# Performance work log

Measured on AMD Instinct MI355X. Metric: run time of the kernel, lower is better.

Reference implementation:

```python
import jax, jax.numpy as jnp
import numpy as np

N, E, IN, H, B, R, ND, K, ER = 50000, 800000, 256, 256, 256, 8, 5000, 16, 20000
LAM = 0.7


def _gat(x, src, dst, W, a_src, a_dst, b):
    """Single-head PyG-style GATConv, add_self_loops=False."""
    h = x @ W                                   # [N,H]
    s = (h @ a_src)[src] + (h @ a_dst)[dst]     # [E]
    e = jax.nn.leaky_relu(s, 0.2)
    m = jax.ops.segment_max(e, dst, num_segments=N)
    m = jnp.where(jnp.isneginf(m), 0.0, m)
    p = jnp.exp(e - m[dst])
    z = jax.ops.segment_sum(p, dst, num_segments=N)
    alpha = p / (z[dst] + 1e-16)                # softmax over incoming edges
    out = jax.ops.segment_sum(alpha[:, None] * h[src], dst, num_segments=N)
    return out + b


def setup_inputs() -> dict:
    key = jax.random.key(0)
    ks = jax.random.split(key, 20)
    d = {}
    d['x'] = jax.random.normal(ks[0], (N, IN), dtype=jnp.float32)
    d['edge_index'] = jax.random.randint(ks[1], (2, E), 0, N)
    d['head_indices'] = jax.random.randint(ks[2], (B,), 0, N)
    d['rel_types'] = jax.random.randint(ks[3], (B,), 0, R)
    d['tail_indices'] = jax.random.randint(ks[4], (B,), 0, N)
    d['g2l'] = jax.random.randint(ks[5], (N,), 0, ND)
    d['rel_edge_src'] = jax.random.randint(ks[6], (3, ER), 0, ND)
    d['sim_neighbors'] = jax.random.randint(ks[7], (ND, K), 0, N)
    d['sim_weights'] = jax.random.uniform(ks[8], (ND, K), dtype=jnp.float32) / K
    sc1 = 1.0 / np.sqrt(IN)
    sc2 = 1.0 / np.sqrt(H)
    d['W1'] = jax.random.normal(ks[9], (IN, H), dtype=jnp.float32) * sc1
    d['a1_src'] = jax.random.normal(ks[10], (H,), dtype=jnp.float32) * sc2
    d['a1_dst'] = jax.random.normal(ks[11], (H,), dtype=jnp.float32) * sc2
    d['b1'] = jnp.zeros((H,), dtype=jnp.float32)
    d['W2'] = jax.random.normal(ks[12], (H, H), dtype=jnp.float32) * sc2
    d['a2_src'] = jax.random.normal(ks[13], (H,), dtype=jnp.float32) * sc2
    d['a2_dst'] = jax.random.normal(ks[14], (H,), dtype=jnp.float32) * sc2
    d['b2'] = jnp.zeros((H,), dtype=jnp.float32)
    d['rel_emb'] = jax.random.normal(ks[15], (R, H), dtype=jnp.float32) * sc2
    return d


def reference(x, edge_index, head_indices, rel_types, tail_indices, g2l,
              rel_edge_src, sim_neighbors, sim_weights,
              W1, a1_src, a1_dst, b1, W2, a2_src, a2_dst, b2, rel_emb):
    src, dst = edge_index[0], edge_index[1]
    # Encoder: GAT -> SiLU -> GAT
    h = _gat(x, src, dst, W1, a1_src, a1_dst, b1)
    h = jax.nn.silu(h)
    node_emb = _gat(h, src, dst, W2, a2_src, a2_dst, b2)  # [N,H]

    # Sequential per-triplet disease-embedding modification (rel 4/5/6)
    def step(emb, tr):
        hi, r = tr
        is_dis = (r >= 4) & (r <= 6)
        ridx = jnp.clip(r - 4, 0, 2)
        local = g2l[hi]
        deg = jnp.sum(rel_edge_src[ridx] == local).astype(emb.dtype)
        c = LAM * jnp.exp(-LAM * deg) + 0.2
        nb = sim_neighbors[local]           # [K]
        w = sim_weights[local]              # [K]
        vec = (w[:, None] * emb[nb]).sum(0)  # weighted neighbor mix
        new = c * vec + (1.0 - c) * emb[hi]
        row = jnp.where(is_dis, new, emb[hi])
        return emb.at[hi].set(row), None

    node_emb, _ = jax.lax.scan(step, node_emb, (head_indices, rel_types))

    # DistMult decode
    head = node_emb[head_indices]
    tail = node_emb[tail_indices]
    rel = rel_emb[rel_types]
    score = (head * rel * tail).sum(-1)
    return jax.nn.sigmoid(score)
```

## Files before the change

### kernel.cpp

```cpp
#include <hip/hip_runtime.h>
#include <cstdint>

#define N_NODES 50000
#define N_EDGES 800000
#define DIM     256
#define BSZ     256
#define ND_     5000
#define KNB     16
#define ER_     20000
#define LAM     0.7f

typedef unsigned int uint;
typedef unsigned short ushort;
typedef __attribute__((ext_vector_type(8))) short bf16x8;
typedef __attribute__((ext_vector_type(4))) float f32x4;

#define MTILES_PAD 3128
#define NB_SCAN    ((N_NODES + 255) / 256)

__device__ __forceinline__ ushort f2bf(float f) {
    uint u = __float_as_uint(f);
    uint r = u + 0x7FFFu + ((u >> 16) & 1u);
    return (ushort)(r >> 16);
}
__device__ __forceinline__ float bflo(uint u) { return __uint_as_float(u << 16); }
__device__ __forceinline__ float bfhi(uint u) { return __uint_as_float(u & 0xffff0000u); }


__device__ __forceinline__ bf16x8 make_af_f32(const float* __restrict__ A,
                                              int row, int c0, int M) {
    float4 v0 = make_float4(0.f, 0.f, 0.f, 0.f);
    float4 v1 = make_float4(0.f, 0.f, 0.f, 0.f);
    if (row < M) {
        v0 = *(const float4*)(A + (size_t)row * 256 + c0);
        v1 = *(const float4*)(A + (size_t)row * 256 + c0 + 16);
    }
    uint4 o;
    o.x = (uint)f2bf(v0.x) | ((uint)f2bf(v0.y) << 16);
    o.y = (uint)f2bf(v0.z) | ((uint)f2bf(v0.w) << 16);
    o.z = (uint)f2bf(v1.x) | ((uint)f2bf(v1.y) << 16);
    o.w = (uint)f2bf(v1.z) | ((uint)f2bf(v1.w) << 16);
    return *(bf16x8*)&o;
}
__device__ __forceinline__ bf16x8 make_af_bf16(const ushort* __restrict__ A,
                                               int row, int c0, int M) {
    uint2 v0 = make_uint2(0u, 0u), v1 = make_uint2(0u, 0u);
    if (row < M) {
        v0 = *(const uint2*)(A + (size_t)row * 256 + c0);
        v1 = *(const uint2*)(A + (size_t)row * 256 + c0 + 16);
    }
    uint4 o; o.x = v0.x; o.y = v0.y; o.z = v1.x; o.w = v1.y;
    return *(bf16x8*)&o;
}

__global__ __launch_bounds__(256)
void pack_b_kernel(const float* __restrict__ W, ushort* __restrict__ out) {
    const int nt = blockIdx.x;
    const int t  = threadIdx.x;
    const int l  = t & 63;
    const int kt0 = (t >> 6) * 2;
    const int n  = nt * 16 + (l & 15);
    const int lg = l >> 4;
#pragma unroll
    for (int p = 0; p < 2; ++p) {
        int kt = kt0 + p;
        ushort us[8];
#pragma unroll
        for (int j = 0; j < 8; ++j) {
            int kk = (j & 3) + lg * 4 + (j >> 2) * 16;
            us[j] = f2bf(W[(size_t)(kt * 32 + kk) * 256 + n]);
        }
        ushort* dst = out + ((size_t)(nt * 8 + kt) * 64 + l) * 8;
        *(uint4*)dst = *(uint4*)us;
    }
}

template<int SRCF32>
__global__ __launch_bounds__(256)
void gemm_bf16_kernel(const float* __restrict__ Af, const ushort* __restrict__ Ab,
                      const ushort* __restrict__ Bp, ushort* __restrict__ H,
                      const float* __restrict__ a_src, const float* __restrict__ a_dst,
                      float* __restrict__ hs, float* __restrict__ hd, int M) {
    __shared__ float sdS[4][64];
    __shared__ float sdD[4][64];
    const int t = threadIdx.x;
    const int w = t >> 6;
    const int l = t & 63;
    const int mt0 = blockIdx.x * 4;
    const int cb  = (l & 15);
    const int lg  = l >> 4;
    f32x4 acc[4][4];
#pragma unroll
    for (int i = 0; i < 4; ++i)
#pragma unroll
        for (int j = 0; j < 4; ++j) acc[i][j] = (f32x4){0.f, 0.f, 0.f, 0.f};

    for (int kt = 0; kt < 8; ++kt) {
        bf16x8 af[4], bfr[4];
        const int c0 = kt * 32 + lg * 4;
#pragma unroll
        for (int mi = 0; mi < 4; ++mi) {
            int row = (mt0 + mi) * 16 + cb;
            af[mi] = SRCF32 ? make_af_f32(Af, row, c0, M)
                            : make_af_bf16(Ab, row, c0, M);
        }
#pragma unroll
        for (int ni = 0; ni < 4; ++ni)
            bfr[ni] = *(const bf16x8*)(Bp + ((size_t)((w * 4 + ni) * 8 + kt) * 64 + l) * 8);
#pragma unroll
        for (int mi = 0; mi < 4; ++mi)
#pragma unroll
            for (int ni = 0; ni < 4; ++ni)
                acc[mi][ni] = __builtin_amdgcn_mfma_f32_16x16x32_bf16(
                    af[mi], bfr[ni], acc[mi][ni], 0, 0, 0);
    }
    const int rbase = (l >> 4) * 4;
    float asv[4], adv[4];
#pragma unroll
    for (int ni = 0; ni < 4; ++ni) {
        int col = (w * 4 + ni) * 16 + cb;
        asv[ni] = a_src[col];
        adv[ni] = a_dst[col];
    }
#pragma unroll
    for (int mi = 0; mi < 4; ++mi) {
#pragma unroll
        for (int r = 0; r < 4; ++r) {
            int row = (mt0 + mi) * 16 + rbase + r;
            float ps = 0.f, pd = 0.f;
#pragma unroll
            for (int ni = 0; ni < 4; ++ni) {
                float hv = acc[mi][ni][r];
                ps = fmaf(hv, asv[ni], ps);
                pd = fmaf(hv, adv[ni], pd);
                if (row < M) {
                    int col = (w * 4 + ni) * 16 + cb;
                    H[(size_t)row * 256 + col] = f2bf(hv);
                }
            }
#pragma unroll
            for (int o = 1; o < 16; o <<= 1) {
                ps += __shfl_xor(ps, o);
                pd += __shfl_xor(pd, o);
            }
            if (cb == 0) {
                sdS[w][mi * 16 + rbase + r] = ps;
                sdD[w][mi * 16 + rbase + r] = pd;
            }
        }
    }
    __syncthreads();
    if (t < 64) {
        int row = mt0 * 16 + t;
        if (row < M) {
            hs[row] = sdS[0][t] + sdS[1][t] + sdS[2][t] + sdS[3][t];
            hd[row] = sdD[0][t] + sdD[1][t] + sdD[2][t] + sdD[3][t];
        }
    }
}

__global__ __launch_bounds__(256)
void hist_kernel(const int* __restrict__ ei, int* __restrict__ deg) {
    int e = blockIdx.x * 256 + threadIdx.x;
    if (e < N_EDGES) atomicAdd(&deg[ei[N_EDGES + e]], 1);
}

__global__ __launch_bounds__(256)
void blockscan_kernel(const int* __restrict__ deg, int* __restrict__ off,
                      int* __restrict__ bsum) {
    __shared__ int s[256];
    const int b = blockIdx.x, t = threadIdx.x;
    const int idx = b * 256 + t;
    int v = (idx < N_NODES) ? deg[idx] : 0;
    s[t] = v;
    __syncthreads();
    for (int o = 1; o < 256; o <<= 1) {
        int x = (t >= o) ? s[t - o] : 0;
        __syncthreads();
        s[t] += x;
        __syncthreads();
    }
    if (idx < N_NODES) off[idx] = s[t] - v;
    if (t == 255) bsum[b] = s[255];
}

__global__ __launch_bounds__(256)
void scan_bsum_kernel(const int* __restrict__ bsum, int* __restrict__ bpre) {
    __shared__ int s[256];
    const int t = threadIdx.x;
    int v = (t < NB_SCAN) ? bsum[t] : 0;
    s[t] = v;
    __syncthreads();
    for (int o = 1; o < 256; o <<= 1) {
        int x = (t >= o) ? s[t - o] : 0;
        __syncthreads();
        s[t] += x;
        __syncthreads();
    }
    if (t < NB_SCAN) bpre[t] = s[t] - v;
}

__global__ __launch_bounds__(256)
void add_offsets_kernel(int* __restrict__ off, const int* __restrict__ bpre) {
    const int b = blockIdx.x, t = threadIdx.x;
    const int idx = b * 256 + t;
    if (idx < N_NODES) off[idx] += bpre[b];
}

__global__ __launch_bounds__(256)
void scatter_kernel(const int* __restrict__ ei, int* __restrict__ off,
                    int* __restrict__ csr_src) {
    int e = blockIdx.x * 256 + threadIdx.x;
    if (e >= N_EDGES) return;
    int d = ei[N_EDGES + e];
    int pos = atomicAdd(&off[d], 1);
    csr_src[pos] = ei[e];
}

__global__ __launch_bounds__(256)
void gat_aggr_kernel(const int* __restrict__ off, const int* __restrict__ csr_src,
                     const float* __restrict__ hs, const float* __restrict__ hd,
                     const ushort* __restrict__ hb, const float* __restrict__ bias,
                     float* __restrict__ out_f32, ushort* __restrict__ out_bf,
                     int do_silu) {
    const int d = blockIdx.x * 4 + (threadIdx.x >> 6);
    const int l = threadIdx.x & 63;
    if (d >= N_NODES) return;
    const int beg = d ? off[d - 1] : 0;
    const int end = off[d];
    const float hdd = hd[d];

    float acc0 = 0.f, acc1 = 0.f, acc2 = 0.f, acc3 = 0.f;
    float zl = 0.f;
    const ushort* __restrict__ hcol = hb + l * 4;

    for (int c0 = beg; c0 < end; c0 += 64) {
        const int cn = min(end - c0, 64);
        int s = 0; float pexp = 0.f;
        if (l < cn) {
            s = csr_src[c0 + l];
            float v = hs[s] + hdd;
            v = (v >= 0.f) ? v : 0.2f * v;
            pexp = __expf(v);
        }
        zl += pexp;
        const int nb4 = cn & ~3;
        int j = 0;
        if (nb4) {
            int s0 = __shfl(s, 0), s1 = __shfl(s, 1), s2 = __shfl(s, 2), s3 = __shfl(s, 3);
            uint2 r0 = *(const uint2*)(hcol + (size_t)s0 * DIM);
            uint2 r1 = *(const uint2*)(hcol + (size_t)s1 * DIM);
            uint2 r2 = *(const uint2*)(hcol + (size_t)s2 * DIM);
            uint2 r3 = *(const uint2*)(hcol + (size_t)s3 * DIM);
            for (j = 4; j < nb4; j += 4) {
                int sn0 = __shfl(s, j),     sn1 = __shfl(s, j + 1);
                int sn2 = __shfl(s, j + 2), sn3 = __shfl(s, j + 3);
                uint2 q0 = *(const uint2*)(hcol + (size_t)sn0 * DIM);
                uint2 q1 = *(const uint2*)(hcol + (size_t)sn1 * DIM);
                uint2 q2 = *(const uint2*)(hcol + (size_t)sn2 * DIM);
                uint2 q3 = *(const uint2*)(hcol + (size_t)sn3 * DIM);
                float p0 = __shfl(pexp, j - 4), p1 = __shfl(pexp, j - 3);
                float p2 = __shfl(pexp, j - 2), p3 = __shfl(pexp, j - 1);
                acc0 = fmaf(p0, bflo(r0.x), acc0); acc1 = fmaf(p0, bfhi(r0.x), acc1);
                acc2 = fmaf(p0, bflo(r0.y), acc2); acc3 = fmaf(p0, bfhi(r0.y), acc3);
                acc0 = fmaf(p1, bflo(r1.x), acc0); acc1 = fmaf(p1, bfhi(r1.x), acc1);
                acc2 = fmaf(p1, bflo(r1.y), acc2); acc3 = fmaf(p1, bfhi(r1.y), acc3);
                acc0 = fmaf(p2, bflo(r2.x), acc0); acc1 = fmaf(p2, bfhi(r2.x), acc1);
                acc2 = fmaf(p2, bflo(r2.y), acc2); acc3 = fmaf(p2, bfhi(r2.y), acc3);
                acc0 = fmaf(p3, bflo(r3.x), acc0); acc1 = fmaf(p3, bfhi(r3.x), acc1);
                acc2 = fmaf(p3, bflo(r3.y), acc2); acc3 = fmaf(p3, bfhi(r3.y), acc3);
                r0 = q0; r1 = q1; r2 = q2; r3 = q3;
            }
            float p0 = __shfl(pexp, j - 4), p1 = __shfl(pexp, j - 3);
            float p2 = __shfl(pexp, j - 2), p3 = __shfl(pexp, j - 1);
            acc0 = fmaf(p0, bflo(r0.x), acc0); acc1 = fmaf(p0, bfhi(r0.x), acc1);
            acc2 = fmaf(p0, bflo(r0.y), acc2); acc3 = fmaf(p0, bfhi(r0.y), acc3);
            acc0 = fmaf(p1, bflo(r1.x), acc0); acc1 = fmaf(p1, bfhi(r1.x), acc1);
            acc2 = fmaf(p1, bflo(r1.y), acc2); acc3 = fmaf(p1, bfhi(r1.y), acc3);
            acc0 = fmaf(p2, bflo(r2.x), acc0); acc1 = fmaf(p2, bfhi(r2.x), acc1);
            acc2 = fmaf(p2, bflo(r2.y), acc2); acc3 = fmaf(p2, bfhi(r2.y), acc3);
            acc0 = fmaf(p3, bflo(r3.x), acc0); acc1 = fmaf(p3, bfhi(r3.x), acc1);
            acc2 = fmaf(p3, bflo(r3.y), acc2); acc3 = fmaf(p3, bfhi(r3.y), acc3);
        }
        for (; j < cn; ++j) {
            int   sj = __shfl(s, j);
            float pj = __shfl(pexp, j);
            uint2 rv = *(const uint2*)(hcol + (size_t)sj * DIM);
            acc0 = fmaf(pj, bflo(rv.x), acc0); acc1 = fmaf(pj, bfhi(rv.x), acc1);
            acc2 = fmaf(pj, bflo(rv.y), acc2); acc3 = fmaf(pj, bfhi(rv.y), acc3);
        }
    }
    float z = zl;
#pragma unroll
    for (int o = 32; o; o >>= 1) z += __shfl_xor(z, o);
    const float inv = (end > beg) ? 1.f / (z + 1e-16f) : 0.f;
    float4 bb = *(const float4*)(bias + l * 4);
    float o0 = acc0 * inv + bb.x;
    float o1 = acc1 * inv + bb.y;
    float o2 = acc2 * inv + bb.z;
    float o3 = acc3 * inv + bb.w;
    if (do_silu) {
        o0 = o0 / (1.f + __expf(-o0));
        o1 = o1 / (1.f + __expf(-o1));
        o2 = o2 / (1.f + __expf(-o2));
        o3 = o3 / (1.f + __expf(-o3));
    }
    if (out_bf) {
        ushort us[4] = {f2bf(o0), f2bf(o1), f2bf(o2), f2bf(o3)};
        *(uint2*)(out_bf + (size_t)d * DIM + l * 4) = *(uint2*)us;
    } else {
        *(float4*)(out_f32 + (size_t)d * DIM + l * 4) = make_float4(o0, o1, o2, o3);
    }
}

__global__ __launch_bounds__(256)
void rel_hist_kernel(const int* __restrict__ res, int* __restrict__ rhist) {
    int i = blockIdx.x * 256 + threadIdx.x;
    if (i < 3 * ER_) atomicAdd(&rhist[(i / ER_) * ND_ + res[i]], 1);
}

__global__ __launch_bounds__(256)
void conflict_kernel(const int* __restrict__ head, const int* __restrict__ rel,
                     const int* __restrict__ g2l, const int* __restrict__ nbs,
                     int* __restrict__ flags) {
    int b = blockIdx.x;
    int rb = rel[b];
    if (rb < 4 || rb > 6) return;
    __shared__ int rd[KNB + 1];
    int t = threadIdx.x;
    if (t == 0) rd[KNB] = head[b];
    if (t < KNB) rd[t] = nbs[(size_t)g2l[head[b]] * KNB + t];
    __syncthreads();
    int rt = rel[t];
    int w = (t != b && rt >= 4 && rt <= 6) ? head[t] : -1;
    if (w >= 0) {
        bool hit = false;
#pragma unroll
        for (int k = 0; k <= KNB; ++k) hit |= (rd[k] == w);
        if (hit) { flags[b] = 1; flags[t] = 1; }
    }
}

__global__ __launch_bounds__(256)
void apply_kernel(float* __restrict__ emb, const int* __restrict__ head,
                  const int* __restrict__ rel, const int* __restrict__ g2l,
                  const int* __restrict__ nbs, const float* __restrict__ wts,
                  const int* __restrict__ rhist, const int* __restrict__ flags) {
    const int t = threadIdx.x;
    if (blockIdx.x < BSZ) {
        int b = blockIdx.x;
        int r = rel[b];
        if (r < 4 || r > 6) return;
        if (flags[b]) return;
        int hi = head[b];
        int local = g2l[hi];
        int dg = rhist[(r - 4) * ND_ + local];
        float c = LAM * __expf(-LAM * (float)dg) + 0.2f;
        const int* __restrict__ nb = nbs + (size_t)local * KNB;
        const float* __restrict__ w = wts + (size_t)local * KNB;
        float v0 = 0.f, v1 = 0.f;
#pragma unroll
        for (int k = 0; k < KNB; k += 2) {
            v0 = fmaf(w[k],     emb[(size_t)nb[k] * DIM + t],     v0);
            v1 = fmaf(w[k + 1], emb[(size_t)nb[k + 1] * DIM + t], v1);
        }
        size_t idx = (size_t)hi * DIM + t;
        emb[idx] = c * (v0 + v1) + (1.f - c) * emb[idx];
        return;
    }
    __shared__ int   snb[BSZ][KNB];
    __shared__ float sw[BSZ][KNB];
    __shared__ int   sh[BSZ];
    __shared__ float sc[BSZ];
    __shared__ int   sf[BSZ];
    int r = rel[t];
    int dis = (r >= 4 && r <= 6);
    int hi = head[t];
    sh[t] = hi;
    sf[t] = dis ? flags[t] : 0;
    if (dis) {
        int local = g2l[hi];
        int dg = rhist[(r - 4) * ND_ + local];
        sc[t] = LAM * __expf(-LAM * (float)dg) + 0.2f;
#pragma unroll
        for (int k = 0; k < KNB; ++k) {
            snb[t][k] = nbs[(size_t)local * KNB + k];
            sw[t][k]  = wts[(size_t)local * KNB + k];
        }
    }
    __syncthreads();
    for (int b = 0; b < BSZ; ++b) {
        if (sf[b]) {
            int hh = sh[b];
            float c = sc[b];
            float v0 = 0.f, v1 = 0.f;
#pragma unroll
            for (int k = 0; k < KNB; k += 2) {
                v0 = fmaf(sw[b][k],     emb[(size_t)snb[b][k] * DIM + t],     v0);
                v1 = fmaf(sw[b][k + 1], emb[(size_t)snb[b][k + 1] * DIM + t], v1);
            }
            size_t idx = (size_t)hh * DIM + t;
            emb[idx] = c * (v0 + v1) + (1.f - c) * emb[idx];
        }
    }
}

__global__ __launch_bounds__(256)
void decode_kernel(const float* __restrict__ emb, const int* __restrict__ head,
                   const int* __restrict__ rel, const int* __restrict__ tail,
                   const float* __restrict__ rel_emb, float* __restrict__ out) {
    int b = blockIdx.x, t = threadIdx.x;
    float v = emb[(size_t)head[b] * DIM + t] *
              rel_emb[(size_t)rel[b] * DIM + t] *
              emb[(size_t)tail[b] * DIM + t];
    __shared__ float red[4];
#pragma unroll
    for (int off = 32; off; off >>= 1) v += __shfl_down(v, off);
    int lane = t & 63, w = t >> 6;
    if (lane == 0) red[w] = v;
    __syncthreads();
    if (t == 0) {
        float s = red[0] + red[1] + red[2] + red[3];
        out[b] = 1.f / (1.f + expf(-s));
    }
}

extern "C" void kernel_launch(void* const* d_in, const int* in_sizes, int n_in,
                              void* d_out, int out_size, void* d_ws, size_t ws_size,
                              hipStream_t stream) {
    const float* x        = (const float*)d_in[0];
    const int*   ei       = (const int*)d_in[1];
    const int*   head     = (const int*)d_in[2];
    const int*   rel      = (const int*)d_in[3];
    const int*   tail     = (const int*)d_in[4];
    const int*   g2l      = (const int*)d_in[5];
    const int*   res      = (const int*)d_in[6];
    const int*   nbs      = (const int*)d_in[7];
    const float* wts      = (const float*)d_in[8];
    const float* W1       = (const float*)d_in[9];
    const float* a1s      = (const float*)d_in[10];
    const float* a1d      = (const float*)d_in[11];
    const float* b1       = (const float*)d_in[12];
    const float* W2       = (const float*)d_in[13];
    const float* a2s      = (const float*)d_in[14];
    const float* a2d      = (const float*)d_in[15];
    const float* b2       = (const float*)d_in[16];
    const float* rel_emb  = (const float*)d_in[17];
    float* out = (float*)d_out;

    char* ws = (char*)d_ws;
    size_t off_b = 0;
    auto alloc = [&](size_t bytes) {
        void* pp = ws + off_b;
        off_b += (bytes + 255) & ~(size_t)255;
        return pp;
    };
    float*  bufB    = (float*)alloc((size_t)N_NODES * DIM * 4);
    ushort* hb      = (ushort*)alloc((size_t)N_NODES * DIM * 2);
    ushort* h1b     = (ushort*)alloc((size_t)N_NODES * DIM * 2);
    float*  hs      = (float*)alloc((size_t)N_NODES * 4);
    float*  hd      = (float*)alloc((size_t)N_NODES * 4);
    size_t z0 = off_b;
    int*    deg     = (int*)alloc((size_t)N_NODES * 4);
    int*    rhist   = (int*)alloc((size_t)3 * ND_ * 4);
    int*    flags   = (int*)alloc((size_t)BSZ * 4);
    size_t z1 = off_b;
    int*    offs    = (int*)alloc((size_t)(N_NODES + 1) * 4);
    int*    csr_src = (int*)alloc((size_t)N_EDGES * 4);
    int*    bsum    = (int*)alloc((size_t)NB_SCAN * 4);
    int*    bpre    = (int*)alloc((size_t)NB_SCAN * 4);
    ushort* wpack1  = (ushort*)alloc((size_t)256 * 256 * 2);
    ushort* wpack2  = (ushort*)alloc((size_t)256 * 256 * 2);

    const int edgeBlocks = (N_EDGES + 255) / 256;
    const int gemmBlocks = MTILES_PAD / 4;
    const int nodeBlocks4 = (N_NODES + 3) / 4;

    hipMemsetAsync(ws + z0, 0, z1 - z0, stream);
    hist_kernel<<<edgeBlocks, 256, 0, stream>>>(ei, deg);
    blockscan_kernel<<<NB_SCAN, 256, 0, stream>>>(deg, offs, bsum);
    scan_bsum_kernel<<<1, 256, 0, stream>>>(bsum, bpre);
    add_offsets_kernel<<<NB_SCAN, 256, 0, stream>>>(offs, bpre);
    scatter_kernel<<<edgeBlocks, 256, 0, stream>>>(ei, offs, csr_src);
    pack_b_kernel<<<16, 256, 0, stream>>>(W1, wpack1);
    pack_b_kernel<<<16, 256, 0, stream>>>(W2, wpack2);
    rel_hist_kernel<<<(3 * ER_ + 255) / 256, 256, 0, stream>>>(res, rhist);

    gemm_bf16_kernel<1><<<gemmBlocks, 256, 0, stream>>>(x, nullptr, wpack1, hb,
                                                        a1s, a1d, hs, hd, N_NODES);
    gat_aggr_kernel<<<nodeBlocks4, 256, 0, stream>>>(offs, csr_src, hs, hd, hb, b1,
                                                     nullptr, h1b, 1);

    gemm_bf16_kernel<0><<<gemmBlocks, 256, 0, stream>>>(nullptr, h1b, wpack2, hb,
                                                        a2s, a2d, hs, hd, N_NODES);
    gat_aggr_kernel<<<nodeBlocks4, 256, 0, stream>>>(offs, csr_src, hs, hd, hb, b2,
                                                     bufB, nullptr, 0);

    conflict_kernel<<<BSZ, 256, 0, stream>>>(head, rel, g2l, nbs, flags);
    apply_kernel<<<BSZ + 1, 256, 0, stream>>>(bufB, head, rel, g2l, nbs, wts,
                                              rhist, flags);
    decode_kernel<<<BSZ, 256, 0, stream>>>(bufB, head, rel, tail, rel_emb, out);
}
```

Before: 439.6 us.

## Stage GEMM A tiles in swizzled LDS, merge prep kernels, keep CSR offsets intact

The GEMM now loads each 64-row A tile cooperatively into a XOR-swizzled LDS buffer with coalesced wide loads, then feeds MFMA fragments from LDS instead of per-lane strided global reads. The weight packing, relation histogram and degree histogram launches are merged into one prep kernel to cut launch count. CSR scatter now uses a separate counter array so offsets stay as exclusive-scan starts with an end sentinel. The aggregation inner loop also drops its software-pipelined prefetch in favour of a simpler loop. The LDS staging adds shared memory use and a barrier per block.

```diff
diff --git a/kernel.cpp b/kernel.cpp
--- a/kernel.cpp
+++ b/kernel.cpp
@@ -15,8 +15,11 @@
 typedef __attribute__((ext_vector_type(8))) short bf16x8;
 typedef __attribute__((ext_vector_type(4))) float f32x4;
 
-#define MTILES_PAD 3128
 #define NB_SCAN    ((N_NODES + 255) / 256)
+#define GROWS      64
+#define GEMM_BLKS  ((N_NODES + GROWS - 1) / GROWS)
+#define RH_BLKS    ((3 * ER_ + 255) / 256)
+#define HIST_BLKS  ((N_EDGES + 255) / 256)
 
 __device__ __forceinline__ ushort f2bf(float f) {
     uint u = __float_as_uint(f);
@@ -27,36 +30,8 @@
 __device__ __forceinline__ float bfhi(uint u) { return __uint_as_float(u & 0xffff0000u); }
 
 
-__device__ __forceinline__ bf16x8 make_af_f32(const float* __restrict__ A,
-                                              int row, int c0, int M) {
-    float4 v0 = make_float4(0.f, 0.f, 0.f, 0.f);
-    float4 v1 = make_float4(0.f, 0.f, 0.f, 0.f);
-    if (row < M) {
-        v0 = *(const float4*)(A + (size_t)row * 256 + c0);
-        v1 = *(const float4*)(A + (size_t)row * 256 + c0 + 16);
-    }
-    uint4 o;
-    o.x = (uint)f2bf(v0.x) | ((uint)f2bf(v0.y) << 16);
-    o.y = (uint)f2bf(v0.z) | ((uint)f2bf(v0.w) << 16);
-    o.z = (uint)f2bf(v1.x) | ((uint)f2bf(v1.y) << 16);
-    o.w = (uint)f2bf(v1.z) | ((uint)f2bf(v1.w) << 16);
-    return *(bf16x8*)&o;
-}
-__device__ __forceinline__ bf16x8 make_af_bf16(const ushort* __restrict__ A,
-                                               int row, int c0, int M) {
-    uint2 v0 = make_uint2(0u, 0u), v1 = make_uint2(0u, 0u);
-    if (row < M) {
-        v0 = *(const uint2*)(A + (size_t)row * 256 + c0);
-        v1 = *(const uint2*)(A + (size_t)row * 256 + c0 + 16);
-    }
-    uint4 o; o.x = v0.x; o.y = v0.y; o.z = v1.x; o.w = v1.y;
-    return *(bf16x8*)&o;
-}
-
-__global__ __launch_bounds__(256)
-void pack_b_kernel(const float* __restrict__ W, ushort* __restrict__ out) {
-    const int nt = blockIdx.x;
-    const int t  = threadIdx.x;
+__device__ __forceinline__ void pack_b_body(const float* __restrict__ W,
+                                            ushort* __restrict__ out, int nt, int t) {
     const int l  = t & 63;
     const int kt0 = (t >> 6) * 2;
     const int n  = nt * 16 + (l & 15);
@@ -70,25 +45,73 @@
             int kk = (j & 3) + lg * 4 + (j >> 2) * 16;
             us[j] = f2bf(W[(size_t)(kt * 32 + kk) * 256 + n]);
         }
-        ushort* dst = out + ((size_t)(nt * 8 + kt) * 64 + l) * 8;
-        *(uint4*)dst = *(uint4*)us;
-    }
+        *(uint4*)(out + ((size_t)(nt * 8 + kt) * 64 + l) * 8) = *(uint4*)us;
+    }
+}
+
+__global__ __launch_bounds__(256)
+void prep_kernel(const float* __restrict__ W1, const float* __restrict__ W2,
+                 ushort* __restrict__ wp1, ushort* __restrict__ wp2,
+                 const int* __restrict__ res, int* __restrict__ rhist,
+                 const int* __restrict__ ei, int* __restrict__ deg) {
+    const int b = blockIdx.x, t = threadIdx.x;
+    if (b < 16)       { pack_b_body(W1, wp1, b, t);      return; }
+    if (b < 32)       { pack_b_body(W2, wp2, b - 16, t); return; }
+    if (b < 32 + RH_BLKS) {
+        int i = (b - 32) * 256 + t;
+        if (i < 3 * ER_) atomicAdd(&rhist[(i / ER_) * ND_ + res[i]], 1);
+        return;
+    }
+    int e = (b - 32 - RH_BLKS) * 256 + t;
+    if (e < N_EDGES) atomicAdd(&deg[ei[N_EDGES + e]], 1);
 }
 
 template<int SRCF32>
 __global__ __launch_bounds__(256)
-void gemm_bf16_kernel(const float* __restrict__ Af, const ushort* __restrict__ Ab,
-                      const ushort* __restrict__ Bp, ushort* __restrict__ H,
-                      const float* __restrict__ a_src, const float* __restrict__ a_dst,
-                      float* __restrict__ hs, float* __restrict__ hd, int M) {
+void gemm_fused_kernel(const float* __restrict__ Af, const ushort* __restrict__ Ab,
+                       const ushort* __restrict__ Bp, ushort* __restrict__ H,
+                       const float* __restrict__ a_src, const float* __restrict__ a_dst,
+                       float* __restrict__ hs, float* __restrict__ hd, int M) {
+    __shared__ uint2 lda[GROWS * 64];
     __shared__ float sdS[4][64];
     __shared__ float sdD[4][64];
     const int t = threadIdx.x;
     const int w = t >> 6;
     const int l = t & 63;
-    const int mt0 = blockIdx.x * 4;
-    const int cb  = (l & 15);
-    const int lg  = l >> 4;
+    const int rb = blockIdx.x * GROWS;
+
+    if (SRCF32) {
+#pragma unroll
+        for (int u = 0; u < 16; ++u) {
+            int f = t + u * 256;
+            int r = f >> 6;
+            int cq = f & 63;
+            int grow = rb + r;
+            float4 v = (grow < M) ? *(const float4*)(Af + (size_t)grow * 256 + cq * 4)
+                                  : make_float4(0.f, 0.f, 0.f, 0.f);
+            uint2 o;
+            o.x = (uint)f2bf(v.x) | ((uint)f2bf(v.y) << 16);
+            o.y = (uint)f2bf(v.z) | ((uint)f2bf(v.w) << 16);
+            lda[r * 64 + (cq ^ (r & 15))] = o;
+        }
+    } else {
+#pragma unroll
+        for (int u = 0; u < 8; ++u) {
+            int f = t + u * 256;
+            int r = f >> 5;
+            int p = f & 31;
+            int grow = rb + r;
+            uint4 v = (grow < M) ? *(const uint4*)(Ab + (size_t)grow * 256 + p * 8)
+                                 : make_uint4(0u, 0u, 0u, 0u);
+            int c = p * 2;
+            lda[r * 64 + ( c      ^ (r & 15))] = make_uint2(v.x, v.y);
+            lda[r * 64 + ((c + 1) ^ (r & 15))] = make_uint2(v.z, v.w);
+        }
+    }
+    __syncthreads();
+
+    const int cb = l & 15;
+    const int lg = l >> 4;
     f32x4 acc[4][4];
 #pragma unroll
     for (int i = 0; i < 4; ++i)
@@ -97,12 +120,13 @@
 
     for (int kt = 0; kt < 8; ++kt) {
         bf16x8 af[4], bfr[4];
-        const int c0 = kt * 32 + lg * 4;
 #pragma unroll
         for (int mi = 0; mi < 4; ++mi) {
-            int row = (mt0 + mi) * 16 + cb;
-            af[mi] = SRCF32 ? make_af_f32(Af, row, c0, M)
-                            : make_af_bf16(Ab, row, c0, M);
+            int row = mi * 16 + cb;
+            uint2 lo = lda[row * 64 + ((kt * 8 + lg)     ^ cb)];
+            uint2 hi = lda[row * 64 + ((kt * 8 + lg + 4) ^ cb)];
+            uint4 cmb; cmb.x = lo.x; cmb.y = lo.y; cmb.z = hi.x; cmb.w = hi.y;
+            af[mi] = *(bf16x8*)&cmb;
         }
 #pragma unroll
         for (int ni = 0; ni < 4; ++ni)
@@ -114,6 +138,7 @@
                 acc[mi][ni] = __builtin_amdgcn_mfma_f32_16x16x32_bf16(
                     af[mi], bfr[ni], acc[mi][ni], 0, 0, 0);
     }
+
     const int rbase = (l >> 4) * 4;
     float asv[4], adv[4];
 #pragma unroll
@@ -126,7 +151,7 @@
     for (int mi = 0; mi < 4; ++mi) {
 #pragma unroll
         for (int r = 0; r < 4; ++r) {
-            int row = (mt0 + mi) * 16 + rbase + r;
+            int row = rb + mi * 16 + rbase + r;
             float ps = 0.f, pd = 0.f;
 #pragma unroll
             for (int ni = 0; ni < 4; ++ni) {
@@ -151,18 +176,12 @@
     }
     __syncthreads();
     if (t < 64) {
-        int row = mt0 * 16 + t;
+        int row = rb + t;
         if (row < M) {
             hs[row] = sdS[0][t] + sdS[1][t] + sdS[2][t] + sdS[3][t];
             hd[row] = sdD[0][t] + sdD[1][t] + sdD[2][t] + sdD[3][t];
         }
     }
-}
-
-__global__ __launch_bounds__(256)
-void hist_kernel(const int* __restrict__ ei, int* __restrict__ deg) {
-    int e = blockIdx.x * 256 + threadIdx.x;
-    if (e < N_EDGES) atomicAdd(&deg[ei[N_EDGES + e]], 1);
 }
 
 __global__ __launch_bounds__(256)
@@ -198,6 +217,7 @@
         __syncthreads();
     }
     if (t < NB_SCAN) bpre[t] = s[t] - v;
+    if (t == 255) bpre[NB_SCAN] = s[255];
 }
 
 __global__ __launch_bounds__(256)
@@ -205,16 +225,17 @@
     const int b = blockIdx.x, t = threadIdx.x;
     const int idx = b * 256 + t;
     if (idx < N_NODES) off[idx] += bpre[b];
-}
-
-__global__ __launch_bounds__(256)
-void scatter_kernel(const int* __restrict__ ei, int* __restrict__ off,
-                    int* __restrict__ csr_src) {
+    if (b == NB_SCAN - 1 && t == 255) off[N_NODES] = bpre[NB_SCAN];
+}
+
+__global__ __launch_bounds__(256)
+void scatter_kernel(const int* __restrict__ ei, const int* __restrict__ off,
+                    int* __restrict__ cnt, int* __restrict__ csr_src) {
     int e = blockIdx.x * 256 + threadIdx.x;
     if (e >= N_EDGES) return;
     int d = ei[N_EDGES + e];
-    int pos = atomicAdd(&off[d], 1);
-    csr_src[pos] = ei[e];
+    int pos = atomicAdd(&cnt[d], 1);
+    csr_src[off[d] + pos] = ei[e];
 }
 
 __global__ __launch_bounds__(256)
@@ -226,8 +247,7 @@
     const int d = blockIdx.x * 4 + (threadIdx.x >> 6);
     const int l = threadIdx.x & 63;
     if (d >= N_NODES) return;
-    const int beg = d ? off[d - 1] : 0;
-    const int end = off[d];
+    const int beg = off[d], end = off[d + 1];
     const float hdd = hd[d];
 
     float acc0 = 0.f, acc1 = 0.f, acc2 = 0.f, acc3 = 0.f;
@@ -244,35 +264,16 @@
             pexp = __expf(v);
         }
         zl += pexp;
-        const int nb4 = cn & ~3;
         int j = 0;
-        if (nb4) {
-            int s0 = __shfl(s, 0), s1 = __shfl(s, 1), s2 = __shfl(s, 2), s3 = __shfl(s, 3);
+        for (; j + 4 <= cn; j += 4) {
+            int   s0 = __shfl(s, j),     s1 = __shfl(s, j + 1);
+            int   s2 = __shfl(s, j + 2), s3 = __shfl(s, j + 3);
+            float p0 = __shfl(pexp, j),     p1 = __shfl(pexp, j + 1);
+            float p2 = __shfl(pexp, j + 2), p3 = __shfl(pexp, j + 3);
             uint2 r0 = *(const uint2*)(hcol + (size_t)s0 * DIM);
             uint2 r1 = *(const uint2*)(hcol + (size_t)s1 * DIM);
             uint2 r2 = *(const uint2*)(hcol + (size_t)s2 * DIM);
             uint2 r3 = *(const uint2*)(hcol + (size_t)s3 * DIM);
-            for (j = 4; j < nb4; j += 4) {
-                int sn0 = __shfl(s, j),     sn1 = __shfl(s, j + 1);
-                int sn2 = __shfl(s, j + 2), sn3 = __shfl(s, j + 3);
-                uint2 q0 = *(const uint2*)(hcol + (size_t)sn0 * DIM);
-                uint2 q1 = *(const uint2*)(hcol + (size_t)sn1 * DIM);
-                uint2 q2 = *(const uint2*)(hcol + (size_t)sn2 * DIM);
-                uint2 q3 = *(const uint2*)(hcol + (size_t)sn3 * DIM);
-                float p0 = __shfl(pexp, j - 4), p1 = __shfl(pexp, j - 3);
-                float p2 = __shfl(pexp, j - 2), p3 = __shfl(pexp, j - 1);
-                acc0 = fmaf(p0, bflo(r0.x), acc0); acc1 = fmaf(p0, bfhi(r0.x), acc1);
-                acc2 = fmaf(p0, bflo(r0.y), acc2); acc3 = fmaf(p0, bfhi(r0.y), acc3);
-                acc0 = fmaf(p1, bflo(r1.x), acc0); acc1 = fmaf(p1, bfhi(r1.x), acc1);
-                acc2 = fmaf(p1, bflo(r1.y), acc2); acc3 = fmaf(p1, bfhi(r1.y), acc3);
-                acc0 = fmaf(p2, bflo(r2.x), acc0); acc1 = fmaf(p2, bfhi(r2.x), acc1);
-                acc2 = fmaf(p2, bflo(r2.y), acc2); acc3 = fmaf(p2, bfhi(r2.y), acc3);
-                acc0 = fmaf(p3, bflo(r3.x), acc0); acc1 = fmaf(p3, bfhi(r3.x), acc1);
-                acc2 = fmaf(p3, bflo(r3.y), acc2); acc3 = fmaf(p3, bfhi(r3.y), acc3);
-                r0 = q0; r1 = q1; r2 = q2; r3 = q3;
-            }
-            float p0 = __shfl(pexp, j - 4), p1 = __shfl(pexp, j - 3);
-            float p2 = __shfl(pexp, j - 2), p3 = __shfl(pexp, j - 1);
             acc0 = fmaf(p0, bflo(r0.x), acc0); acc1 = fmaf(p0, bfhi(r0.x), acc1);
             acc2 = fmaf(p0, bflo(r0.y), acc2); acc3 = fmaf(p0, bfhi(r0.y), acc3);
             acc0 = fmaf(p1, bflo(r1.x), acc0); acc1 = fmaf(p1, bfhi(r1.x), acc1);
@@ -311,12 +312,6 @@
     } else {
         *(float4*)(out_f32 + (size_t)d * DIM + l * 4) = make_float4(o0, o1, o2, o3);
     }
-}
-
-__global__ __launch_bounds__(256)
-void rel_hist_kernel(const int* __restrict__ res, int* __restrict__ rhist) {
-    int i = blockIdx.x * 256 + threadIdx.x;
-    if (i < 3 * ER_) atomicAdd(&rhist[(i / ER_) * ND_ + res[i]], 1);
 }
 
 __global__ __launch_bounds__(256)
@@ -462,36 +457,34 @@
     float*  hd      = (float*)alloc((size_t)N_NODES * 4);
     size_t z0 = off_b;
     int*    deg     = (int*)alloc((size_t)N_NODES * 4);
+    int*    cnt     = (int*)alloc((size_t)N_NODES * 4);
     int*    rhist   = (int*)alloc((size_t)3 * ND_ * 4);
     int*    flags   = (int*)alloc((size_t)BSZ * 4);
     size_t z1 = off_b;
     int*    offs    = (int*)alloc((size_t)(N_NODES + 1) * 4);
     int*    csr_src = (int*)alloc((size_t)N_EDGES * 4);
     int*    bsum    = (int*)alloc((size_t)NB_SCAN * 4);
-    int*    bpre    = (int*)alloc((size_t)NB_SCAN * 4);
+    int*    bpre    = (int*)alloc((size_t)(NB_SCAN + 1) * 4);
     ushort* wpack1  = (ushort*)alloc((size_t)256 * 256 * 2);
     ushort* wpack2  = (ushort*)alloc((size_t)256 * 256 * 2);
 
-    const int edgeBlocks = (N_EDGES + 255) / 256;
-    const int gemmBlocks = MTILES_PAD / 4;
     const int nodeBlocks4 = (N_NODES + 3) / 4;
+    const int prepBlocks  = 32 + RH_BLKS + HIST_BLKS;
 
     hipMemsetAsync(ws + z0, 0, z1 - z0, stream);
-    hist_kernel<<<edgeBlocks, 256, 0, stream>>>(ei, deg);
+    prep_kernel<<<prepBlocks, 256, 0, stream>>>(W1, W2, wpack1, wpack2,
+                                                res, rhist, ei, deg);
     blockscan_kernel<<<NB_SCAN, 256, 0, stream>>>(deg, offs, bsum);
     scan_bsum_kernel<<<1, 256, 0, stream>>>(bsum, bpre);
     add_offsets_kernel<<<NB_SCAN, 256, 0, stream>>>(offs, bpre);
-    scatter_kernel<<<edgeBlocks, 256, 0, stream>>>(ei, offs, csr_src);
-    pack_b_kernel<<<16, 256, 0, stream>>>(W1, wpack1);
-    pack_b_kernel<<<16, 256, 0, stream>>>(W2, wpack2);
-    rel_hist_kernel<<<(3 * ER_ + 255) / 256, 256, 0, stream>>>(res, rhist);
-
-    gemm_bf16_kernel<1><<<gemmBlocks, 256, 0, stream>>>(x, nullptr, wpack1, hb,
+    scatter_kernel<<<HIST_BLKS, 256, 0, stream>>>(ei, offs, cnt, csr_src);
+
+    gemm_fused_kernel<1><<<GEMM_BLKS, 256, 0, stream>>>(x, nullptr, wpack1, hb,
                                                         a1s, a1d, hs, hd, N_NODES);
     gat_aggr_kernel<<<nodeBlocks4, 256, 0, stream>>>(offs, csr_src, hs, hd, hb, b1,
                                                      nullptr, h1b, 1);
 
-    gemm_bf16_kernel<0><<<gemmBlocks, 256, 0, stream>>>(nullptr, h1b, wpack2, hb,
+    gemm_fused_kernel<0><<<GEMM_BLKS, 256, 0, stream>>>(nullptr, h1b, wpack2, hb,
                                                         a2s, a2d, hs, hd, N_NODES);
     gat_aggr_kernel<<<nodeBlocks4, 256, 0, stream>>>(offs, csr_src, hs, hd, hb, b2,
                                                      bufB, nullptr, 0);
```

New measurement: 397.8 us. -9.5%, faster.
